# Performance work log

Hardware: AMD Instinct MI355X
Metric: run time of the kernel (lower is better)

Reference implementation:

```python
import jax, jax.numpy as jnp
import numpy as np

ALPHA, BETA, LAMB = 1.0, 1.0, 1e-4
K, TAU, DELTA = 16, 0.1, 1e-4
N, D, B, NQ = 100000, 256, 256, 4096


def setup_inputs() -> dict:
    key = jax.random.key(0)
    k1, k2, k3, k4, k5, k6 = jax.random.split(key, 6)
    X = jax.random.normal(k1, (N, D), dtype=jnp.float32)
    W = jax.random.normal(k2, (D, D), dtype=jnp.float32) / np.sqrt(D)
    q_batch = jax.random.normal(k3, (B, D), dtype=jnp.float32)
    pre_weights = jax.random.uniform(k4, (NQ, K), dtype=jnp.float32)
    pre_weights = pre_weights / pre_weights.sum(axis=1, keepdims=True)
    q_indices = jax.random.randint(k5, (B,), 0, NQ)
    pre_indices = jax.random.randint(k6, (NQ, K), 0, N)
    return {"X": X, "W": W, "q_batch": q_batch, "pre_weights": pre_weights,
            "q_indices": q_indices, "pre_indices": pre_indices}


def _matrix_sqrt(A):
    # differentiable symmetric matrix sqrt via eigendecomposition
    w, v = jnp.linalg.eigh(A)
    w = jnp.sqrt(jnp.clip(w, 0.0))
    return (v * w) @ v.T


def _loss_dist(T, mu_X, cov_X, cov_X_sqrt):
    mu = jnp.mean(T, axis=0)
    Tc = T - mu
    cov = Tc.T @ Tc / T.shape[0] + DELTA * jnp.eye(T.shape[1], dtype=T.dtype)
    loss_mean = jnp.sum((mu - mu_X) ** 2)
    cov_sqrt = _matrix_sqrt(cov)
    sqrt_term = _matrix_sqrt(cov_sqrt @ cov_X @ cov_sqrt)
    loss_cov = jnp.trace(cov_X + cov - 2.0 * sqrt_term)
    return jnp.clip(loss_mean + loss_cov, 0.0)


def _kl_per_sample(pre_idx, pre_w, post_idx, post_w):
    # union via first-occurrence mask over concatenated candidates [2K]
    cand = jnp.concatenate([pre_idx, post_idx])
    eq = cand[:, None] == cand[None, :]
    first = ~jnp.tril(eq, k=-1).any(axis=1)
    p = (cand[:, None] == pre_idx[None, :]).astype(pre_w.dtype) @ pre_w
    q = (cand[:, None] == post_idx[None, :]).astype(post_w.dtype) @ post_w
    p = jnp.where(first, jnp.clip(p, 1e-8), 0.0)
    p = p / p.sum()
    q = jnp.where(first, jnp.clip(q, 1e-8), 0.0)
    q = q / q.sum()
    logp = jnp.log(jnp.where(first, p, 1.0))
    logq = jnp.log(jnp.where(first, q, 1.0))
    return jnp.sum(jnp.where(first, p * (logp - logq), 0.0))


def _forward(X, W, q_batch, pre_weights, q_indices, pre_indices):
    # precomputed database stats
    mu_X = jnp.mean(X, axis=0)
    Xc = X - mu_X
    cov_X = Xc.T @ Xc / X.shape[0] + DELTA * jnp.eye(X.shape[1], dtype=X.dtype)
    cov_X_sqrt = _matrix_sqrt(cov_X)

    T = q_batch @ W  # model(q_batch): [B, D]

    loss_dist = _loss_dist(T, mu_X, cov_X, cov_X_sqrt)

    # brute-force exact KNN (faiss flat L2) on detached T
    Td = jax.lax.stop_gradient(T)
    d2 = (jnp.sum(Td * Td, axis=1, keepdims=True)
          - 2.0 * (Td @ X.T) + jnp.sum(X * X, axis=1))  # [B, N]
    _, post_idx = jax.lax.top_k(-d2, K)  # [B, K]

    X_nb = X[post_idx]  # [B, K, D]
    l2 = jnp.sum((T[:, None, :] - X_nb) ** 2, axis=-1)  # [B, K], with grad
    post_w = jax.nn.softmax(-l2 / TAU, axis=1)

    pre_idx_b = pre_indices[q_indices]   # [B, K]
    pre_w_b = pre_weights[q_indices]     # [B, K]
    kls = jax.vmap(_kl_per_sample)(pre_idx_b, pre_w_b, post_idx, post_w)
    loss_knn = jnp.mean(kls)

    loss_reg = 0.5 * jnp.sum(W ** 2)

    total = ALPHA * loss_dist + BETA * loss_knn + LAMB * loss_reg
    return total, loss_dist, loss_knn


def reference(X, W, q_batch, pre_weights, q_indices, pre_indices):
    return _forward(X, W, q_batch, pre_weights, q_indices, pre_indices)
```

## Files before the change

### kernel.cpp

```cpp
#include <hip/hip_runtime.h>

#define NPTS   100000
#define DIMD   256
#define BQ     256
#define PCHUNK 128
#define NPCH   782
#define NCAND  (NPCH*16)
#define NS_ITERS 26
#define KSPLIT  32
#define KSLICE  3136
#define KS2    576
#define NZ2    175

#define SC_LM   0
#define SC_TRCX 1
#define SC_TRCT 2
#define SC_FROB 3
#define SC_KNN  4
#define SC_REG  5
#define SC_LD   6

#define BIGF 3.4e38f

typedef __attribute__((ext_vector_type(4))) float f32x4;
typedef __attribute__((ext_vector_type(8))) unsigned short u16x8;
typedef __attribute__((ext_vector_type(8))) __bf16 bf16x8;

static __device__ __forceinline__ unsigned short f2bf(float f) {
    unsigned u = __float_as_uint(f);
    unsigned r = (u + 0x7fffu + ((u >> 16) & 1u)) >> 16;
    return (unsigned short)r;
}
static __device__ __forceinline__ float bf2f(unsigned short h) {
    return __uint_as_float(((unsigned)h) << 16);
}
static __device__ __forceinline__ unsigned pack_hi(float a, float b) {
    return (__float_as_uint(a) >> 16) | (__float_as_uint(b) & 0xffff0000u);
}
static __device__ __forceinline__ float trunc_bf(float a) {
    return __uint_as_float(__float_as_uint(a) & 0xffff0000u);
}
static __device__ __forceinline__ unsigned short top16(float v) {
    return (unsigned short)(__float_as_uint(v) >> 16);
}
static __device__ __forceinline__ f32x4 mfma16(u16x8 a, u16x8 b, f32x4 c) {
    return __builtin_amdgcn_mfma_f32_16x16x32_bf16(
        __builtin_bit_cast(bf16x8, a), __builtin_bit_cast(bf16x8, b), c, 0, 0, 0);
}

static __device__ __forceinline__ unsigned enc_f32(float f) {
    unsigned u = __float_as_uint(f);
    return u ^ (unsigned)(((int)u >> 31) | 0x80000000);
}
static __device__ __forceinline__ float dec_f32(unsigned e) {
    unsigned u = e ^ ((e & 0x80000000u) ? 0x80000000u : 0xFFFFFFFFu);
    return __uint_as_float(u);
}
static __device__ __forceinline__ unsigned umin32(unsigned a, unsigned b) { return a < b ? a : b; }
static __device__ __forceinline__ void ceu(unsigned& a, unsigned& b) {
    unsigned lo = a < b ? a : b;
    unsigned hi = a < b ? b : a;
    a = lo; b = hi;
}
static __device__ __forceinline__ void sort16(unsigned* r) {
#pragma unroll
    for (int k = 2; k <= 16; k <<= 1)
#pragma unroll
        for (int j = k >> 1; j > 0; j >>= 1)
#pragma unroll
            for (int i = 0; i < 16; ++i) {
                int l = i ^ j;
                if (l > i) {
                    if ((i & k) == 0) ceu(r[i], r[l]);
                    else              ceu(r[l], r[i]);
                }
            }
}
static __device__ __forceinline__ void clean16(unsigned* r) {
#pragma unroll
    for (int j = 8; j > 0; j >>= 1)
#pragma unroll
        for (int i = 0; i < 16; ++i) {
            int l = i ^ j;
            if (l > i) ceu(r[i], r[l]);
        }
}

__global__ __launch_bounds__(256) void zero_kernel(float* ws) {
    int idx = blockIdx.x * 256 + threadIdx.x;
    if (idx < 66560) ws[idx] = 0.0f;
}

__global__ __launch_bounds__(256) void statsx_kernel(const float* __restrict__ X,
                                                     float* __restrict__ xsq,
                                                     float* __restrict__ mu_sum,
                                                     unsigned short* __restrict__ XHs,
                                                     unsigned short* __restrict__ XLs) {
    int w    = threadIdx.x >> 6;
    int lane = threadIdx.x & 63;
    int rbase = blockIdx.x * 512;
    float cs0 = 0.f, cs1 = 0.f, cs2 = 0.f, cs3 = 0.f;
    for (int m = 0; m < 128; ++m) {
        int r = rbase + w + 4 * m;
        if (r < NPTS) {
            float4 v = *(const float4*)&X[r * DIMD + 4 * lane];
            cs0 += v.x; cs1 += v.y; cs2 += v.z; cs3 += v.w;
            float ss = v.x * v.x + v.y * v.y + v.z * v.z + v.w * v.w;
            for (int off = 32; off; off >>= 1) ss += __shfl_down(ss, off);
            if (lane == 0) xsq[r] = ss;
            if (XHs) {
                int g = (lane >> 1) ^ (r & 7);
                int h = lane & 1;
                uint2 hv = { pack_hi(v.x, v.y), pack_hi(v.z, v.w) };
                uint2 lv = { pack_hi(v.x - trunc_bf(v.x), v.y - trunc_bf(v.y)),
                             pack_hi(v.z - trunc_bf(v.z), v.w - trunc_bf(v.w)) };
                *(uint2*)(XHs + (size_t)r * 256 + g * 8 + h * 4) = hv;
                *(uint2*)(XLs + (size_t)r * 256 + g * 8 + h * 4) = lv;
            }
        } else if (XHs) {
            int g = (lane >> 1) ^ (r & 7);
            int h = lane & 1;
            uint2 z2 = {0u, 0u};
            *(uint2*)(XHs + (size_t)r * 256 + g * 8 + h * 4) = z2;
            *(uint2*)(XLs + (size_t)r * 256 + g * 8 + h * 4) = z2;
        }
    }
    atomicAdd(&mu_sum[4 * lane + 0], cs0);
    atomicAdd(&mu_sum[4 * lane + 1], cs1);
    atomicAdd(&mu_sum[4 * lane + 2], cs2);
    atomicAdd(&mu_sum[4 * lane + 3], cs3);
}

__global__ __launch_bounds__(256) void xtk_kernel(const unsigned short* __restrict__ XHs,
                                                  const unsigned short* __restrict__ XLs,
                                                  unsigned short* __restrict__ XTH,
                                                  unsigned short* __restrict__ XTL) {
    __shared__ unsigned short LH[32][268];
    __shared__ unsigned short LL[32][268];
    const int t = threadIdx.x;
#pragma unroll 1
    for (int st = 0; st < 8; ++st) {
        const int r0 = blockIdx.x * 256 + st * 32;
        const int row = t >> 3;
        const int r = r0 + row;
#pragma unroll
        for (int gg = 0; gg < 4; ++gg) {
            int glog = (t & 7) + gg * 8;
            int gphys = glog ^ (r & 7);
            u16x8 h = *(const u16x8*)(XHs + (size_t)r * 256 + gphys * 8);
            u16x8 l = *(const u16x8*)(XLs + (size_t)r * 256 + gphys * 8);
            *(u16x8*)&LH[row][glog * 8] = h;
            *(u16x8*)&LL[row][glog * 8] = l;
        }
        __syncthreads();
        {
            unsigned pk[16];
#pragma unroll
            for (int m = 0; m < 16; ++m)
                pk[m] = (unsigned)LH[2 * m][t] | ((unsigned)LH[2 * m + 1][t] << 16);
            uint4* oh = (uint4*)(XTH + (size_t)t * 100352 + r0);
#pragma unroll
            for (int q = 0; q < 4; ++q)
                oh[q] = make_uint4(pk[4 * q], pk[4 * q + 1], pk[4 * q + 2], pk[4 * q + 3]);
#pragma unroll
            for (int m = 0; m < 16; ++m)
                pk[m] = (unsigned)LL[2 * m][t] | ((unsigned)LL[2 * m + 1][t] << 16);
            uint4* ol = (uint4*)(XTL + (size_t)t * 100352 + r0);
#pragma unroll
            for (int q = 0; q < 4; ++q)
                ol[q] = make_uint4(pk[4 * q], pk[4 * q + 1], pk[4 * q + 2], pk[4 * q + 3]);
        }
        __syncthreads();
    }
}

__global__ __launch_bounds__(256) void covx2_kernel(const unsigned short* __restrict__ XTH,
                                                    const unsigned short* __restrict__ XTL,
                                                    float* __restrict__ acc_out) {
    const int quad = blockIdx.x;
    const int qi = quad >> 1, qj = quad & 1;
    const int t = threadIdx.x, w = t >> 6, lane = t & 63;
    const int l15 = lane & 15, l4 = lane >> 4;
    const int k0 = blockIdx.y * KS2;
    const int kend = (k0 + KS2 < 100352) ? (k0 + KS2) : 100352;
    f32x4 acc[2][8];
#pragma unroll
    for (int f = 0; f < 2; ++f)
#pragma unroll
        for (int cf = 0; cf < 8; ++cf) { f32x4 z = {0.f, 0.f, 0.f, 0.f}; acc[f][cf] = z; }
    const size_t rowA0 = (size_t)(qi * 128 + w * 32 + l15) * 100352;
    const size_t rowA1 = (size_t)(qi * 128 + w * 32 + 16 + l15) * 100352;
#pragma unroll 1
    for (int k = k0; k < kend; k += 32) {
        const int ko = k + l4 * 8;
        u16x8 ah0 = *(const u16x8*)(XTH + rowA0 + ko);
        u16x8 al0 = *(const u16x8*)(XTL + rowA0 + ko);
        u16x8 ah1 = *(const u16x8*)(XTH + rowA1 + ko);
        u16x8 al1 = *(const u16x8*)(XTL + rowA1 + ko);
#pragma unroll
        for (int cf = 0; cf < 8; ++cf) {
            const size_t rb = (size_t)(qj * 128 + cf * 16 + l15) * 100352 + ko;
            u16x8 bh = *(const u16x8*)(XTH + rb);
            u16x8 bl = *(const u16x8*)(XTL + rb);
            acc[0][cf] = mfma16(ah0, bh, acc[0][cf]);
            acc[0][cf] = mfma16(ah0, bl, acc[0][cf]);
            acc[0][cf] = mfma16(al0, bh, acc[0][cf]);
            acc[1][cf] = mfma16(ah1, bh, acc[1][cf]);
            acc[1][cf] = mfma16(ah1, bl, acc[1][cf]);
            acc[1][cf] = mfma16(al1, bh, acc[1][cf]);
        }
    }
#pragma unroll
    for (int f = 0; f < 2; ++f)
#pragma unroll
        for (int cf = 0; cf < 8; ++cf)
#pragma unroll
            for (int i = 0; i < 4; ++i) {
                const int r = qi * 128 + w * 32 + f * 16 + l4 * 4 + i;
                const int c = qj * 128 + cf * 16 + l15;
                atomicAdd(&acc_out[r * DIMD + c], acc[f][cf][i]);
            }
}

__global__ __launch_bounds__(256) void covx_kernel(const float* __restrict__ X,
                                                   float* __restrict__ acc_out) {
    __shared__ float Ais[16][64];
    __shared__ float Ajs[16][64];
    int t = threadIdx.x;
    int i0 = blockIdx.x * 64, j0 = blockIdx.y * 64;
    int ks = blockIdx.z * KSLICE;
    int lr = t >> 4, lc = (t & 15) * 4;
    int tx = t & 15, ty = t >> 4;
    float acc[4][4] = {};
    for (int kb = 0; kb < KSLICE; kb += 16) {
        int k = ks + kb + lr;
        if (k < NPTS) {
            float4 vi = *(const float4*)&X[k * DIMD + i0 + lc];
            float4 vj = *(const float4*)&X[k * DIMD + j0 + lc];
            *(float4*)&Ais[lr][lc] = vi;
            *(float4*)&Ajs[lr][lc] = vj;
        } else {
            float4 z = {0.f, 0.f, 0.f, 0.f};
            *(float4*)&Ais[lr][lc] = z;
            *(float4*)&Ajs[lr][lc] = z;
        }
        __syncthreads();
#pragma unroll
        for (int kk = 0; kk < 16; ++kk) {
            float4 a = *(float4*)&Ais[kk][tx * 4];
            float4 b = *(float4*)&Ajs[kk][ty * 4];
            float av[4] = {a.x, a.y, a.z, a.w};
            float bv[4] = {b.x, b.y, b.z, b.w};
#pragma unroll
            for (int m = 0; m < 4; ++m)
#pragma unroll
                for (int n = 0; n < 4; ++n) acc[m][n] += av[m] * bv[n];
        }
        __syncthreads();
    }
#pragma unroll
    for (int m = 0; m < 4; ++m)
#pragma unroll
        for (int n = 0; n < 4; ++n)
            atomicAdd(&acc_out[(i0 + 4 * tx + m) * DIMD + j0 + 4 * ty + n], acc[m][n]);
}

__global__ __launch_bounds__(256) void covxfin2_kernel(const float* __restrict__ acc,
                                                       const float* __restrict__ mu_sum,
                                                       float* __restrict__ covXf,
                                                       float* __restrict__ scal) {
    int idx = blockIdx.x * 256 + threadIdx.x;
    int i = idx >> 8, j = idx & 255;
    const float invN = 1.0f / (float)NPTS;
    float v = acc[idx] * invN - (mu_sum[i] * invN) * (mu_sum[j] * invN) + ((i == j) ? 1e-4f : 0.0f);
    covXf[idx] = v;
    if (i == j) atomicAdd(&scal[SC_TRCX], v);
}

__global__ __launch_bounds__(256) void mm32_kernel(const float* A, const float* B, float* C, const float* D,
                                                   const float* A2, const float* B2, float* C2, const float* D2,
                                                   int mode, const float* mu, float* scal) {
    __shared__ float As[32][32];
    __shared__ float Bs[32][32];
    __shared__ float red[256];
    int t = threadIdx.x;
    int tx = t & 15, ty = t >> 4;
    int i0 = blockIdx.x * 32, j0 = blockIdx.y * 32;
    int lr = t >> 3, lc = (t & 7) * 4;
    float acc[2][2] = {};
    for (int kb = 0; kb < 256; kb += 32) {
        if (mode == 2) {
            float4 v = *(const float4*)&A[(kb + lr) * DIMD + i0 + lc];
            *(float4*)&As[lr][lc] = v;
        } else {
            float4 v = *(const float4*)&A[(i0 + lr) * DIMD + kb + lc];
            As[lc + 0][lr] = v.x; As[lc + 1][lr] = v.y; As[lc + 2][lr] = v.z; As[lc + 3][lr] = v.w;
        }
        {
            float4 v = *(const float4*)&B[(kb + lr) * DIMD + j0 + lc];
            *(float4*)&Bs[lr][lc] = v;
        }
        __syncthreads();
#pragma unroll
        for (int kk = 0; kk < 32; ++kk) {
            float a0 = As[kk][2 * tx], a1 = As[kk][2 * tx + 1];
            float b0 = Bs[kk][2 * ty], b1 = Bs[kk][2 * ty + 1];
            acc[0][0] += a0 * b0; acc[0][1] += a0 * b1;
            acc[1][0] += a1 * b0; acc[1][1] += a1 * b1;
        }
        __syncthreads();
    }
    float fr = 0.f;
#pragma unroll
    for (int ii = 0; ii < 2; ++ii)
#pragma unroll
        for (int jj = 0; jj < 2; ++jj) {
            int i = i0 + 2 * tx + ii, j = j0 + 2 * ty + jj;
            float v = acc[ii][jj];
            if (mode == 2) {
                v = v * (1.0f / 256.0f) - mu[i] * mu[j] + ((i == j) ? 1e-4f : 0.0f);
                if (i == j) atomicAdd(&scal[SC_TRCT], v);
            }
            C[i * DIMD + j] = v;
            if (mode == 1) fr += v * v;
        }
    if (mode == 0 && C2 != nullptr) {
        unsigned short* TH = (unsigned short*)C2;
        unsigned short* TL = (unsigned short*)const_cast<float*>(D2);
#pragma unroll
        for (int ii = 0; ii < 2; ++ii) {
            int i = i0 + 2 * tx + ii;
            int jc = j0 + 2 * ty;
            float x0 = acc[ii][0], x1 = acc[ii][1];
            *(unsigned*)&TH[i * DIMD + jc] = pack_hi(x0, x1);
            *(unsigned*)&TL[i * DIMD + jc] = pack_hi(x0 - trunc_bf(x0), x1 - trunc_bf(x1));
        }
    }
    if (mode == 1) {
        red[t] = fr; __syncthreads();
        for (int s2 = 128; s2 > 0; s2 >>= 1) { if (t < s2) red[t] += red[t + s2]; __syncthreads(); }
        if (t == 0) atomicAdd(&scal[SC_FROB], red[0]);
    }
}

__global__ __launch_bounds__(256) void tstats_kernel(const float* __restrict__ Tm,
                                                     const float* __restrict__ mu_sum,
                                                     float* __restrict__ mu_T,
                                                     float* __restrict__ scal) {
    __shared__ float red[256];
    int j = threadIdx.x;
    float s = 0.f;
    for (int b = 0; b < BQ; ++b) s += Tm[b * DIMD + j];
    float mt = s * (1.0f / 256.0f);
    mu_T[j] = mt;
    float d = mt - mu_sum[j] * (1.0f / (float)NPTS);
    red[j] = d * d;
    __syncthreads();
    for (int s2 = 128; s2 > 0; s2 >>= 1) { if (j < s2) red[j] += red[j + s2]; __syncthreads(); }
    if (j == 0) scal[SC_LM] = red[0];
}

__global__ __launch_bounds__(256) void inityz2_kernel(const float* __restrict__ G,
                                                      const float* __restrict__ scal,
                                                      float* __restrict__ Y, float* __restrict__ Z,
                                                      unsigned short* __restrict__ YaH,
                                                      unsigned short* __restrict__ YaL,
                                                      unsigned short* __restrict__ ZaH,
                                                      unsigned short* __restrict__ ZaL) {
    int idx = blockIdx.x * 256 + threadIdx.x;
    float invs = rsqrtf(scal[SC_FROB]);
    float y = G[idx] * invs;
    Y[idx] = y;
    YaH[idx] = top16(y);
    YaL[idx] = top16(y - trunc_bf(y));
    bool dg = ((idx >> 8) == (idx & 255));
    Z[idx] = dg ? 1.0f : 0.0f;
    ZaH[idx] = dg ? (unsigned short)0x3F80 : (unsigned short)0;
    ZaL[idx] = 0;
}

__global__ __launch_bounds__(256) void nsfused_kernel(
        const float* __restrict__ Ycur, const float* __restrict__ Zcur,
        const unsigned short* __restrict__ YH, const unsigned short* __restrict__ YL,
        const unsigned short* __restrict__ ZH, const unsigned short* __restrict__ ZL,
        float* __restrict__ Yn, float* __restrict__ Zn,
        unsigned short* __restrict__ YnH, unsigned short* __restrict__ YnL,
        unsigned short* __restrict__ ZnH, unsigned short* __restrict__ ZnL) {
    __shared__ __align__(16) unsigned short VH[32 * 264];
    __shared__ __align__(16) unsigned short VL[32 * 264];
    __shared__ __align__(16) unsigned short IH[32 * 264];
    __shared__ __align__(16) unsigned short IL[32 * 264];
    const int t = threadIdx.x, w = t >> 6, lane = t & 63;
    const int l15 = lane & 15, l4 = lane >> 4;
    const int j0 = blockIdx.x * 32;
    const unsigned short *M1H, *M1L, *M2H, *M2L, *VsH, *VsL;
    const float* Dm; float* Out; unsigned short *OH, *OL;
    if (blockIdx.y == 0) { M1H = ZH; M1L = ZL; M2H = YH; M2L = YL; VsH = YH; VsL = YL;
                           Dm = Ycur; Out = Yn; OH = YnH; OL = YnL; }
    else                 { M1H = YH; M1L = YL; M2H = ZH; M2L = ZL; VsH = ZH; VsL = ZL;
                           Dm = Zcur; Out = Zn; OH = ZnH; OL = ZnL; }
    {
        const int col = t & 31, k0 = (t >> 5) * 32;
#pragma unroll
        for (int m = 0; m < 16; ++m) {
            const int k = k0 + 2 * m;
            unsigned h0 = VsH[(size_t)k * 256 + j0 + col];
            unsigned h1 = VsH[(size_t)(k + 1) * 256 + j0 + col];
            unsigned l0 = VsL[(size_t)k * 256 + j0 + col];
            unsigned l1 = VsL[(size_t)(k + 1) * 256 + j0 + col];
            *(unsigned*)&VH[col * 264 + k] = h0 | (h1 << 16);
            *(unsigned*)&VL[col * 264 + k] = l0 | (l1 << 16);
        }
    }
    __syncthreads();
    f32x4 acc[4][2];
#pragma unroll
    for (int f = 0; f < 4; ++f)
#pragma unroll
        for (int cf = 0; cf < 2; ++cf) { f32x4 z = {0.f, 0.f, 0.f, 0.f}; acc[f][cf] = z; }
#pragma unroll
    for (int ks = 0; ks < 8; ++ks) {
        const int bo0 = l15 * 264 + ks * 32 + l4 * 8;
        const int bo1 = (16 + l15) * 264 + ks * 32 + l4 * 8;
        u16x8 bh0 = *(const u16x8*)&VH[bo0];
        u16x8 bl0 = *(const u16x8*)&VL[bo0];
        u16x8 bh1 = *(const u16x8*)&VH[bo1];
        u16x8 bl1 = *(const u16x8*)&VL[bo1];
#pragma unroll
        for (int f = 0; f < 4; ++f) {
            const size_t ro = (size_t)(w * 64 + f * 16 + l15) * 256 + ks * 32 + l4 * 8;
            u16x8 ah = *(const u16x8*)(M1H + ro);
            u16x8 al = *(const u16x8*)(M1L + ro);
            acc[f][0] = mfma16(ah, bh0, acc[f][0]);
            acc[f][0] = mfma16(ah, bl0, acc[f][0]);
            acc[f][0] = mfma16(al, bh0, acc[f][0]);
            acc[f][1] = mfma16(ah, bh1, acc[f][1]);
            acc[f][1] = mfma16(ah, bl1, acc[f][1]);
            acc[f][1] = mfma16(al, bh1, acc[f][1]);
        }
    }
#pragma unroll
    for (int f = 0; f < 4; ++f)
#pragma unroll
        for (int cf = 0; cf < 2; ++cf) {
            float v0 = acc[f][cf][0], v1 = acc[f][cf][1], v2 = acc[f][cf][2], v3 = acc[f][cf][3];
            unsigned h01 = pack_hi(v0, v1), h23 = pack_hi(v2, v3);
            unsigned l01 = pack_hi(v0 - trunc_bf(v0), v1 - trunc_bf(v1));
            unsigned l23 = pack_hi(v2 - trunc_bf(v2), v3 - trunc_bf(v3));
            const int ad = (cf * 16 + l15) * 264 + w * 64 + f * 16 + l4 * 4;
            *(uint2*)&IH[ad] = make_uint2(h01, h23);
            *(uint2*)&IL[ad] = make_uint2(l01, l23);
        }
    __syncthreads();
#pragma unroll
    for (int f = 0; f < 4; ++f)
#pragma unroll
        for (int cf = 0; cf < 2; ++cf) { f32x4 z = {0.f, 0.f, 0.f, 0.f}; acc[f][cf] = z; }
#pragma unroll
    for (int ks = 0; ks < 8; ++ks) {
        const int bo0 = l15 * 264 + ks * 32 + l4 * 8;
        const int bo1 = (16 + l15) * 264 + ks * 32 + l4 * 8;
        u16x8 bh0 = *(const u16x8*)&IH[bo0];
        u16x8 bl0 = *(const u16x8*)&IL[bo0];
        u16x8 bh1 = *(const u16x8*)&IH[bo1];
        u16x8 bl1 = *(const u16x8*)&IL[bo1];
#pragma unroll
        for (int f = 0; f < 4; ++f) {
            const size_t ro = (size_t)(w * 64 + f * 16 + l15) * 256 + ks * 32 + l4 * 8;
            u16x8 ah = *(const u16x8*)(M2H + ro);
            u16x8 al = *(const u16x8*)(M2L + ro);
            acc[f][0] = mfma16(ah, bh0, acc[f][0]);
            acc[f][0] = mfma16(ah, bl0, acc[f][0]);
            acc[f][0] = mfma16(al, bh0, acc[f][0]);
            acc[f][1] = mfma16(ah, bh1, acc[f][1]);
            acc[f][1] = mfma16(ah, bl1, acc[f][1]);
            acc[f][1] = mfma16(al, bh1, acc[f][1]);
        }
    }
#pragma unroll
    for (int f = 0; f < 4; ++f)
#pragma unroll
        for (int cf = 0; cf < 2; ++cf)
#pragma unroll
            for (int i = 0; i < 4; ++i) {
                const int r = w * 64 + f * 16 + l4 * 4 + i;
                const int c = j0 + cf * 16 + l15;
                float v = 1.5f * Dm[r * 256 + c] - 0.5f * acc[f][cf][i];
                Out[r * 256 + c] = v;
                OH[r * 256 + c] = top16(v);
                OL[r * 256 + c] = top16(v - trunc_bf(v));
            }
}

__global__ __launch_bounds__(256) void findist_kernel(const float* __restrict__ Yfin,
                                                      float* __restrict__ scal) {
    __shared__ float red[256];
    int t = threadIdx.x;
    red[t] = Yfin[t * (DIMD + 1)];
    __syncthreads();
    for (int s2 = 128; s2 > 0; s2 >>= 1) { if (t < s2) red[t] += red[t + s2]; __syncthreads(); }
    if (t == 0) {
        float frobsq = scal[SC_FROB];
        float tr_sqrt = powf(frobsq, 0.25f) * red[0];
        float lc = scal[SC_TRCX] + scal[SC_TRCT] - 2.0f * tr_sqrt;
        scal[SC_LD] = fmaxf(0.0f, scal[SC_LM] + lc);
    }
}

__global__ __launch_bounds__(256) void reg_kernel(const float* __restrict__ W, float* __restrict__ scal) {
    __shared__ float red[256];
    int t = threadIdx.x;
    float s = 0.f;
    int base = blockIdx.x * 1024;
    for (int m = 0; m < 4; ++m) { float w = W[base + m * 256 + t]; s += w * w; }
    red[t] = s;
    __syncthreads();
    for (int s2 = 128; s2 > 0; s2 >>= 1) { if (t < s2) red[t] += red[t + s2]; __syncthreads(); }
    if (t == 0) atomicAdd(&scal[SC_REG], red[0]);
}

__global__ __launch_bounds__(256, 2) void knn3_kernel(const unsigned short* __restrict__ TmH,
                                                      const unsigned short* __restrict__ TmL,
                                                      const unsigned short* __restrict__ XHs,
                                                      const unsigned short* __restrict__ XLs,
                                                      const float* __restrict__ xsq,
                                                      float* __restrict__ ck, int* __restrict__ ci) {
    __shared__ __align__(16) unsigned char sm2[69632];
    unsigned* kt = (unsigned*)(sm2 + 32768);
    const int t = threadIdx.x;
    const int w = t >> 6, lane = t & 63;
    const int l15 = lane & 15, l4 = lane >> 4;
    const int p0 = blockIdx.x * PCHUNK;
    const int swz = (l15 & 7) << 4;

    unsigned sk[16];
#pragma unroll
    for (int s = 0; s < 16; ++s) sk[s] = 0xFFFFFFFFu;

    uint4 ph[4], pl[4];
    {
        const uint4* gh = (const uint4*)(XHs + (size_t)p0 * 256);
        const uint4* gl = (const uint4*)(XLs + (size_t)p0 * 256);
#pragma unroll
        for (int r = 0; r < 4; ++r) { ph[r] = gh[r * 256 + t]; pl[r] = gl[r * 256 + t]; }
    }

#pragma unroll 1
    for (int pc = 0; pc < 4; ++pc) {
        const int pbase = p0 + pc * 32;
#pragma unroll
        for (int r = 0; r < 4; ++r) {
            *(uint4*)(sm2 + (r * 256 + t) * 16) = ph[r];
            *(uint4*)(sm2 + 16384 + (r * 256 + t) * 16) = pl[r];
        }
        __syncthreads();
        f32x4 acc[4][2];
#pragma unroll
        for (int f = 0; f < 4; ++f)
#pragma unroll
            for (int pt = 0; pt < 2; ++pt) { f32x4 z = {0.f, 0.f, 0.f, 0.f}; acc[f][pt] = z; }
#pragma unroll
        for (int ks = 0; ks < 8; ++ks) {
            const int g = (((ks * 4 + l4) << 4)) ^ swz;
            const int b0 = l15 * 512 + g;
            const int b1 = (16 + l15) * 512 + g;
            u16x8 bh0 = *(const u16x8*)(sm2 + b0);
            u16x8 bl0 = *(const u16x8*)(sm2 + 16384 + b0);
            u16x8 bh1 = *(const u16x8*)(sm2 + b1);
            u16x8 bl1 = *(const u16x8*)(sm2 + 16384 + b1);
#pragma unroll
            for (int f = 0; f < 4; ++f) {
                const size_t ro = (size_t)(w * 64 + f * 16 + l15) * 256 + ks * 32 + l4 * 8;
                u16x8 ah = *(const u16x8*)(TmH + ro);
                u16x8 al = *(const u16x8*)(TmL + ro);
                acc[f][0] = mfma16(ah, bh0, acc[f][0]);
                acc[f][0] = mfma16(ah, bl0, acc[f][0]);
                acc[f][0] = mfma16(al, bh0, acc[f][0]);
                acc[f][1] = mfma16(ah, bh1, acc[f][1]);
                acc[f][1] = mfma16(ah, bl1, acc[f][1]);
                acc[f][1] = mfma16(al, bh1, acc[f][1]);
            }
        }
#pragma unroll
        for (int pt = 0; pt < 2; ++pt) {
            const int p = pbase + pt * 16 + l15;
            const float xv = xsq[p];
            const bool ok = (p < NPTS);
            const unsigned lidx = (unsigned)(pc * 32 + pt * 16 + l15);
#pragma unroll
            for (int f = 0; f < 4; ++f)
#pragma unroll
                for (int i = 0; i < 4; ++i) {
                    float d2 = ok ? (xv - 2.0f * acc[f][pt][i]) : BIGF;
                    unsigned e = (enc_f32(d2) & 0xFFFFFF80u) | lidx;
                    kt[(w * 64 + f * 16 + l4 * 4 + i) * 36 + pt * 16 + l15] = e;
                }
        }
        __syncthreads();
        if (pc < 3) {
            const uint4* gh = (const uint4*)(XHs + (size_t)(p0 + (pc + 1) * 32) * 256);
            const uint4* gl = (const uint4*)(XLs + (size_t)(p0 + (pc + 1) * 32) * 256);
#pragma unroll
            for (int r = 0; r < 4; ++r) { ph[r] = gh[r * 256 + t]; pl[r] = gl[r * 256 + t]; }
        }
        {
            unsigned b[32];
#pragma unroll
            for (int c4 = 0; c4 < 8; ++c4) {
                uint4 v = *(const uint4*)(kt + t * 36 + c4 * 4);
                b[c4 * 4 + 0] = v.x; b[c4 * 4 + 1] = v.y;
                b[c4 * 4 + 2] = v.z; b[c4 * 4 + 3] = v.w;
            }
            sort16(b);
            sort16(b + 16);
#pragma unroll
            for (int i = 0; i < 16; ++i) b[i] = umin32(b[i], b[31 - i]);
            clean16(b);
#pragma unroll
            for (int i = 0; i < 16; ++i) sk[i] = umin32(sk[i], b[15 - i]);
            clean16(sk);
        }
    }
    const int base = t * NCAND + blockIdx.x * 16;
#pragma unroll
    for (int s = 0; s < 16; ++s) {
        ck[base + s] = dec_f32(sk[s] & 0xFFFFFF80u);
        ci[base + s] = p0 + (int)(sk[s] & 127u);
    }
}

static __device__ __forceinline__ void knn_load(const float* __restrict__ X, int p0, int pc, int t,
                                                float4 s0[2], float4 s1[2]) {
#pragma unroll
    for (int rep = 0; rep < 2; ++rep) {
        int g = t + rep * 512;
        int row = g >> 5, c0 = (g & 31) * 8;
        int p = p0 + pc * 32 + row;
        if (p < NPTS) {
            s0[rep] = *(const float4*)&X[p * DIMD + c0];
            s1[rep] = *(const float4*)&X[p * DIMD + c0 + 4];
        } else {
            float4 z = {0.f, 0.f, 0.f, 0.f};
            s0[rep] = z; s1[rep] = z;
        }
    }
}
static __device__ __forceinline__ void knn_write(unsigned short* XH, unsigned short* XL, int t,
                                                 const float4 s0[2], const float4 s1[2]) {
#pragma unroll
    for (int rep = 0; rep < 2; ++rep) {
        int g = t + rep * 512;
        int row = g >> 5, c0 = (g & 31) * 8;
        float f[8] = {s0[rep].x, s0[rep].y, s0[rep].z, s0[rep].w,
                      s1[rep].x, s1[rep].y, s1[rep].z, s1[rep].w};
        u16x8 h, lo;
#pragma unroll
        for (int j = 0; j < 8; ++j) {
            unsigned short hb = f2bf(f[j]);
            h[j] = hb;
            lo[j] = f2bf(f[j] - bf2f(hb));
        }
        *(u16x8*)&XH[row * 264 + c0] = h;
        *(u16x8*)&XL[row * 264 + c0] = lo;
    }
}
__global__ __launch_bounds__(512, 2) void knn_kernel(const float* __restrict__ Tm,
                                                     const float* __restrict__ X,
                                                     const float* __restrict__ xsq,
                                                     float* __restrict__ ck, int* __restrict__ ci) {
    __shared__ __align__(16) unsigned char smem[50688];
    unsigned short* XH = (unsigned short*)smem;
    unsigned short* XL = (unsigned short*)(smem + 16896);
    float* ktf = (float*)smem;
    float* tk  = (float*)(smem + 34304);
    int*   ti  = (int*)  (smem + 42496);
    const int t    = threadIdx.x;
    const int w    = t >> 6;
    const int lane = t & 63;
    const int l15  = lane & 15;
    const int l4   = lane >> 4;
    const int p0   = blockIdx.x * PCHUNK;
    const int q0   = blockIdx.y * 128;
    u16x8 aH[8], aL[8];
    {
        const int q = q0 + w * 16 + l15;
        const float* tq = Tm + q * DIMD + l4 * 8;
#pragma unroll
        for (int ks = 0; ks < 8; ++ks) {
            float4 v0 = *(const float4*)(tq + ks * 32);
            float4 v1 = *(const float4*)(tq + ks * 32 + 4);
            float f[8] = {v0.x, v0.y, v0.z, v0.w, v1.x, v1.y, v1.z, v1.w};
            u16x8 h, lo;
#pragma unroll
            for (int j = 0; j < 8; ++j) {
                unsigned short hb = f2bf(f[j]);
                h[j] = hb;
                lo[j] = f2bf(f[j] - bf2f(hb));
            }
            aH[ks] = h; aL[ks] = lo;
        }
    }
    float worst = BIGF; int wslot = 0;
    float4 s0[2], s1[2];
    knn_load(X, p0, 0, t, s0, s1);
    knn_write(XH, XL, t, s0, s1);
#pragma unroll
    for (int h = 0; h < 2; ++h) {
        f32x4 acc[4];
#pragma unroll
        for (int a2 = 0; a2 < 4; ++a2) { f32x4 z = {0.f, 0.f, 0.f, 0.f}; acc[a2] = z; }
#pragma unroll
        for (int pc2 = 0; pc2 < 2; ++pc2) {
            const int pc = 2 * h + pc2;
            __syncthreads();
            if (pc < 3) knn_load(X, p0, pc + 1, t, s0, s1);
#pragma unroll
            for (int ks = 0; ks < 8; ++ks) {
#pragma unroll
                for (int pt = 0; pt < 2; ++pt) {
                    const int off = (pt * 16 + l15) * 264 + ks * 32 + l4 * 8;
                    u16x8 bh = *(const u16x8*)&XH[off];
                    u16x8 bl = *(const u16x8*)&XL[off];
                    acc[pc2 * 2 + pt] = mfma16(aH[ks], bh, acc[pc2 * 2 + pt]);
                    acc[pc2 * 2 + pt] = mfma16(aH[ks], bl, acc[pc2 * 2 + pt]);
                    acc[pc2 * 2 + pt] = mfma16(aL[ks], bh, acc[pc2 * 2 + pt]);
                }
            }
            __syncthreads();
            if (pc2 == 0 && pc < 3) knn_write(XH, XL, t, s0, s1);
        }
#pragma unroll
        for (int pc2 = 0; pc2 < 2; ++pc2) {
#pragma unroll
            for (int pt = 0; pt < 2; ++pt) {
                const int pl = pc2 * 32 + pt * 16 + l15;
                const int p  = p0 + h * 64 + pl;
                const float xv = (p < NPTS) ? xsq[p] : 0.f;
#pragma unroll
                for (int i = 0; i < 4; ++i) {
                    float key = (p < NPTS) ? (xv - 2.0f * acc[pc2 * 2 + pt][i]) : BIGF;
                    ktf[(w * 16 + l4 * 4 + i) * 67 + pl] = key;
                }
            }
        }
        __syncthreads();
        if (t < 128) {
            if (h == 0) {
#pragma unroll
                for (int s = 0; s < 16; ++s) { tk[s * 128 + t] = BIGF; ti[s * 128 + t] = 0x7fffffff; }
            }
            for (int c = 0; c < 64; ++c) {
                float key = ktf[t * 67 + c];
                if (key < worst) {
                    tk[wslot * 128 + t] = key; ti[wslot * 128 + t] = p0 + h * 64 + c;
                    worst = tk[t]; wslot = 0;
#pragma unroll
                    for (int s = 1; s < 16; ++s) {
                        float v = tk[s * 128 + t];
                        if (v > worst) { worst = v; wslot = s; }
                    }
                }
            }
        }
        __syncthreads();
        if (h == 0) knn_write(XH, XL, t, s0, s1);
    }
    if (t < 128) {
        int base = (q0 + t) * NCAND + blockIdx.x * 16;
        for (int s = 0; s < 16; ++s) { ck[base + s] = tk[s * 128 + t]; ci[base + s] = ti[s * 128 + t]; }
    }
}

__global__ __launch_bounds__(256) void merge_kernel(const float* __restrict__ ck,
                                                    const int* __restrict__ ci,
                                                    int* __restrict__ post_idx) {
    __shared__ float tk[16][256];
    __shared__ int   ti[16][256];
    __shared__ float rk[256];
    __shared__ int   ri[256];
    __shared__ int   rt2[256];
    __shared__ int   rs2[256];
    int q = blockIdx.x, t = threadIdx.x;
    for (int s = 0; s < 16; ++s) { tk[s][t] = BIGF; ti[s][t] = 0x7fffffff; }
    float worst = BIGF; int wslot = 0;
    for (int e = t; e < NCAND; e += 256) {
        float key = ck[q * NCAND + e];
        if (key < worst) {
            tk[wslot][t] = key; ti[wslot][t] = ci[q * NCAND + e];
            worst = tk[0][t]; wslot = 0;
            for (int s = 1; s < 16; ++s)
                if (tk[s][t] > worst) { worst = tk[s][t]; wslot = s; }
        }
    }
    __syncthreads();
    for (int r = 0; r < 16; ++r) {
        float bk = tk[0][t]; int bi = ti[0][t], bs = 0;
        for (int s = 1; s < 16; ++s) {
            float k2 = tk[s][t]; int i2 = ti[s][t];
            if (k2 < bk || (k2 == bk && i2 < bi)) { bk = k2; bi = i2; bs = s; }
        }
        rk[t] = bk; ri[t] = bi; rt2[t] = t; rs2[t] = bs;
        __syncthreads();
        for (int s2 = 128; s2 > 0; s2 >>= 1) {
            if (t < s2) {
                float ko = rk[t + s2]; int io = ri[t + s2];
                if (ko < rk[t] || (ko == rk[t] && io < ri[t])) {
                    rk[t] = ko; ri[t] = io; rt2[t] = rt2[t + s2]; rs2[t] = rs2[t + s2];
                }
            }
            __syncthreads();
        }
        if (t == rt2[0]) { tk[rs2[0]][t] = BIGF; ti[rs2[0]][t] = 0x7fffffff; }
        if (t == 0) post_idx[q * 16 + r] = ri[0];
        __syncthreads();
    }
}

__global__ __launch_bounds__(256) void l2sm_kernel(const float* __restrict__ Tm,
                                                   const float* __restrict__ X,
                                                   const int* __restrict__ post_idx,
                                                   float* __restrict__ post_w) {
    __shared__ float l2s[16];
    int b = blockIdx.x, t = threadIdx.x;
    int k = t >> 4, j = t & 15;
    int idx = post_idx[b * 16 + k];
    float s = 0.f;
    for (int i = 0; i < 16; ++i) {
        int d = j + 16 * i;
        float df = Tm[b * DIMD + d] - X[idx * DIMD + d];
        s += df * df;
    }
    for (int off = 8; off; off >>= 1) s += __shfl_down(s, off, 16);
    if (j == 0) l2s[k] = s;
    __syncthreads();
    if (t < 16) {
        float x = -l2s[t] * 10.0f;
        float m = x;
        for (int mm = 8; mm; mm >>= 1) m = fmaxf(m, __shfl_xor(m, mm, 16));
        float e = expf(x - m);
        float ssum = e;
        for (int mm = 8; mm; mm >>= 1) ssum += __shfl_xor(ssum, mm, 16);
        post_w[b * 16 + t] = e / ssum;
    }
}

__global__ __launch_bounds__(256) void kl_kernel(const int* __restrict__ q_indices,
                                                 const int* __restrict__ pre_indices,
                                                 const float* __restrict__ pre_weights,
                                                 const int* __restrict__ post_idx,
                                                 const float* __restrict__ post_w,
                                                 float* __restrict__ scal) {
    int b = threadIdx.x;
    int qi = q_indices[b];
    int pid[16]; float pw[16]; int sid[16]; float sw[16];
    for (int k = 0; k < 16; ++k) {
        pid[k] = pre_indices[qi * 16 + k];
        pw[k]  = pre_weights[qi * 16 + k];
        sid[k] = post_idx[b * 16 + k];
        sw[k]  = post_w[b * 16 + k];
    }
    float psum = 0.f, qsum = 0.f, kl = 0.f;
    for (int pass = 0; pass < 2; ++pass) {
        for (int i = 0; i < 32; ++i) {
            int c = (i < 16) ? pid[i] : sid[i - 16];
            bool first = true;
            for (int jj = 0; jj < i; ++jj) {
                int cj = (jj < 16) ? pid[jj] : sid[jj - 16];
                if (cj == c) { first = false; break; }
            }
            if (!first) continue;
            float p = 0.f, q = 0.f;
            for (int k2 = 0; k2 < 16; ++k2) {
                if (pid[k2] == c) p += pw[k2];
                if (sid[k2] == c) q += sw[k2];
            }
            p = fmaxf(p, 1e-8f); q = fmaxf(q, 1e-8f);
            if (pass == 0) { psum += p; qsum += q; }
            else {
                float pn = p / psum, qn = q / qsum;
                kl += pn * (logf(pn) - logf(qn));
            }
        }
    }
    atomicAdd(&scal[SC_KNN], kl * (1.0f / 256.0f));
}

__global__ void assemble_kernel(const float* __restrict__ scal, float* __restrict__ out) {
    if (threadIdx.x == 0) {
        float ld = scal[SC_LD], lk = scal[SC_KNN], reg = scal[SC_REG];
        out[0] = ld + lk + 1e-4f * 0.5f * reg;
        out[1] = ld;
        out[2] = lk;
    }
}

extern "C" void kernel_launch(void* const* d_in, const int* in_sizes, int n_in,
                              void* d_out, int out_size, void* d_ws, size_t ws_size,
                              hipStream_t stream) {
    (void)in_sizes; (void)n_in; (void)out_size;
    const float* X           = (const float*)d_in[0];
    const float* W           = (const float*)d_in[1];
    const float* q_batch     = (const float*)d_in[2];
    const float* pre_weights = (const float*)d_in[3];
    const int*   q_indices   = (const int*)d_in[4];
    const int*   pre_indices = (const int*)d_in[5];
    float* out = (float*)d_out;
    float* ws  = (float*)d_ws;

    float* mu_sum = ws + 0;
    float* scal   = ws + 256;
    float* mu_T   = ws + 512;
    float* covX   = ws + 1024;
    float* Tm     = ws + 66560;
    float* cov    = ws + 132096;
    float* G      = ws + 197632;
    float* Ya     = ws + 263168;
    float* Za     = ws + 328704;
    float* Yb     = ws + 394240;
    float* Zb     = ws + 459776;
    float* covXf  = ws + 525312;
    float* xsq    = ws + 590848;
    float* post_w = ws + 691200;
    int*   post_idx = (int*)(ws + 695296);
    float* ck     = ws + 699392;
    int*   ci     = (int*)(ws + 3902464);
    unsigned short* YaH = (unsigned short*)(ws + 699392);
    unsigned short* YaL = (unsigned short*)(ws + 732160);
    unsigned short* ZaH = (unsigned short*)(ws + 764928);
    unsigned short* ZaL = (unsigned short*)(ws + 797696);
    unsigned short* YbH = (unsigned short*)(ws + 830464);
    unsigned short* YbL = (unsigned short*)(ws + 863232);
    unsigned short* ZbH = (unsigned short*)(ws + 896000);
    unsigned short* ZbL = (unsigned short*)(ws + 928768);
    unsigned short* XHs = (unsigned short*)(ws + 7105536);
    unsigned short* XLs = (unsigned short*)(ws + 19950592);
    unsigned short* TmH = (unsigned short*)(ws + 32795648);
    unsigned short* TmL = (unsigned short*)(ws + 32828416);
    unsigned short* XTH = (unsigned short*)(ws + 32845824);
    unsigned short* XTL = (unsigned short*)(ws + 45690880);
    const bool haveIMG = (ws_size >= (size_t)131444736);
    const bool haveXT  = (ws_size >= (size_t)234143744);

    zero_kernel<<<260, 256, 0, stream>>>(ws);
    reg_kernel<<<64, 256, 0, stream>>>(W, scal);
    statsx_kernel<<<196, 256, 0, stream>>>(X, xsq, mu_sum,
                                           haveIMG ? XHs : nullptr, haveIMG ? XLs : nullptr);
    if (haveXT) {
        xtk_kernel<<<392, 256, 0, stream>>>(XHs, XLs, XTH, XTL);
        covx2_kernel<<<dim3(4, NZ2), 256, 0, stream>>>(XTH, XTL, covX);
    } else {
        covx_kernel<<<dim3(4, 4, KSPLIT), 256, 0, stream>>>(X, covX);
    }
    covxfin2_kernel<<<256, 256, 0, stream>>>(covX, mu_sum, covXf, scal);
    mm32_kernel<<<dim3(8, 8, 1), 256, 0, stream>>>(q_batch, W, Tm, nullptr,
                                                   nullptr, nullptr,
                                                   haveIMG ? (float*)TmH : nullptr,
                                                   haveIMG ? (float*)TmL : nullptr, 0, nullptr, scal);
    tstats_kernel<<<1, 256, 0, stream>>>(Tm, mu_sum, mu_T, scal);
    mm32_kernel<<<dim3(8, 8, 1), 256, 0, stream>>>(Tm, Tm, cov, nullptr,
                                                   nullptr, nullptr, nullptr, nullptr, 2, mu_T, scal);
    mm32_kernel<<<dim3(8, 8, 1), 256, 0, stream>>>(cov, covXf, G, nullptr,
                                                   nullptr, nullptr, nullptr, nullptr, 1, nullptr, scal);
    if (haveIMG) {
        knn3_kernel<<<NPCH, 256, 0, stream>>>(TmH, TmL, XHs, XLs, xsq, ck, ci);
    } else {
        knn_kernel<<<dim3(NPCH, 2, 1), 512, 0, stream>>>(Tm, X, xsq, ck, ci);
    }
    merge_kernel<<<256, 256, 0, stream>>>(ck, ci, post_idx);
    l2sm_kernel<<<256, 256, 0, stream>>>(Tm, X, post_idx, post_w);
    kl_kernel<<<1, 256, 0, stream>>>(q_indices, pre_indices, pre_weights, post_idx, post_w, scal);
    inityz2_kernel<<<256, 256, 0, stream>>>(G, scal, Ya, Za, YaH, YaL, ZaH, ZaL);
    {
        float *Yc = Ya, *Zc = Za, *Yn = Yb, *Zn = Zb;
        unsigned short *cYH = YaH, *cYL = YaL, *cZH = ZaH, *cZL = ZaL;
        unsigned short *nYH = YbH, *nYL = YbL, *nZH = ZbH, *nZL = ZbL;
        for (int it = 0; it < NS_ITERS; ++it) {
            nsfused_kernel<<<dim3(8, 2), 256, 0, stream>>>(Yc, Zc, cYH, cYL, cZH, cZL,
                                                           Yn, Zn, nYH, nYL, nZH, nZL);
            float* tf;
            tf = Yc; Yc = Yn; Yn = tf;
            tf = Zc; Zc = Zn; Zn = tf;
            unsigned short* tu;
            tu = cYH; cYH = nYH; nYH = tu;
            tu = cYL; cYL = nYL; nYL = tu;
            tu = cZH; cZH = nZH; nZH = tu;
            tu = cZL; cZL = nZL; nZL = tu;
        }
        findist_kernel<<<1, 256, 0, stream>>>(Yc, scal);
    }
    assemble_kernel<<<1, 64, 0, stream>>>(scal, out);
}
```

Baseline: 1.704 ms.

## Rework statsx, Newton-Schulz, knn3 tiling and add per-query merge kernel

Splits statsx over four times more blocks, halves the column tile of the fused Newton-Schulz kernel so it launches 32 blocks instead of 16, and changes knn3 to load X tiles directly instead of register-prefetching them. knn3 now also sorts its 32 candidate keys as two separate 16-element halves merged into the running top-16. A new merge2 kernel runs one block per query, doing a per-thread insertion top-16 followed by a shared-memory tree reduction. The aim is more parallelism on the latency-bound small kernels, but knn3 loses its load/compute overlap and merge2 depends on early exit in the sorted runs.

```diff
diff --git a/kernel.cpp b/kernel.cpp
--- a/kernel.cpp
+++ b/kernel.cpp
@@ -85,6 +85,24 @@
             if (l > i) ceu(r[i], r[l]);
         }
 }
+static __device__ __forceinline__ int lessp(float ka, int ia, float kb, int ib) {
+    return (ka < kb) || (ka == kb && ia < ib);
+}
+static __device__ __forceinline__ void ceup(float& ka, int& ia, float& kb, int& ib) {
+    bool sw = lessp(kb, ib, ka, ia);
+    float t0 = sw ? kb : ka, t1 = sw ? ka : kb;
+    int   u0 = sw ? ib : ia, u1 = sw ? ia : ib;
+    ka = t0; kb = t1; ia = u0; ib = u1;
+}
+static __device__ __forceinline__ void cleanp16(float* k, int* i) {
+#pragma unroll
+    for (int j = 8; j > 0; j >>= 1)
+#pragma unroll
+        for (int x = 0; x < 16; ++x) {
+            int l = x ^ j;
+            if (l > x) ceup(k[x], i[x], k[l], i[l]);
+        }
+}
 
 __global__ __launch_bounds__(256) void zero_kernel(float* ws) {
     int idx = blockIdx.x * 256 + threadIdx.x;
@@ -98,9 +116,9 @@
                                                      unsigned short* __restrict__ XLs) {
     int w    = threadIdx.x >> 6;
     int lane = threadIdx.x & 63;
-    int rbase = blockIdx.x * 512;
+    int rbase = blockIdx.x * 128;
     float cs0 = 0.f, cs1 = 0.f, cs2 = 0.f, cs3 = 0.f;
-    for (int m = 0; m < 128; ++m) {
+    for (int m = 0; m < 32; ++m) {
         int r = rbase + w + 4 * m;
         if (r < NPTS) {
             float4 v = *(const float4*)&X[r * DIMD + 4 * lane];
@@ -386,13 +404,13 @@
         float* __restrict__ Yn, float* __restrict__ Zn,
         unsigned short* __restrict__ YnH, unsigned short* __restrict__ YnL,
         unsigned short* __restrict__ ZnH, unsigned short* __restrict__ ZnL) {
-    __shared__ __align__(16) unsigned short VH[32 * 264];
-    __shared__ __align__(16) unsigned short VL[32 * 264];
-    __shared__ __align__(16) unsigned short IH[32 * 264];
-    __shared__ __align__(16) unsigned short IL[32 * 264];
+    __shared__ __align__(16) unsigned short VH[16 * 264];
+    __shared__ __align__(16) unsigned short VL[16 * 264];
+    __shared__ __align__(16) unsigned short IH[16 * 264];
+    __shared__ __align__(16) unsigned short IL[16 * 264];
     const int t = threadIdx.x, w = t >> 6, lane = t & 63;
     const int l15 = lane & 15, l4 = lane >> 4;
-    const int j0 = blockIdx.x * 32;
+    const int j0 = blockIdx.x * 16;
     const unsigned short *M1H, *M1L, *M2H, *M2L, *VsH, *VsL;
     const float* Dm; float* Out; unsigned short *OH, *OL;
     if (blockIdx.y == 0) { M1H = ZH; M1L = ZL; M2H = YH; M2L = YL; VsH = YH; VsL = YL;
@@ -400,9 +418,9 @@
     else                 { M1H = YH; M1L = YL; M2H = ZH; M2L = ZL; VsH = ZH; VsL = ZL;
                            Dm = Zcur; Out = Zn; OH = ZnH; OL = ZnL; }
     {
-        const int col = t & 31, k0 = (t >> 5) * 32;
-#pragma unroll
-        for (int m = 0; m < 16; ++m) {
+        const int col = t >> 4, k0 = (t & 15) * 16;
+#pragma unroll
+        for (int m = 0; m < 8; ++m) {
             const int k = k0 + 2 * m;
             unsigned h0 = VsH[(size_t)k * 256 + j0 + col];
             unsigned h1 = VsH[(size_t)(k + 1) * 256 + j0 + col];
@@ -413,83 +431,63 @@
         }
     }
     __syncthreads();
-    f32x4 acc[4][2];
-#pragma unroll
-    for (int f = 0; f < 4; ++f)
-#pragma unroll
-        for (int cf = 0; cf < 2; ++cf) { f32x4 z = {0.f, 0.f, 0.f, 0.f}; acc[f][cf] = z; }
+    f32x4 acc[4];
+#pragma unroll
+    for (int f = 0; f < 4; ++f) { f32x4 z = {0.f, 0.f, 0.f, 0.f}; acc[f] = z; }
 #pragma unroll
     for (int ks = 0; ks < 8; ++ks) {
-        const int bo0 = l15 * 264 + ks * 32 + l4 * 8;
-        const int bo1 = (16 + l15) * 264 + ks * 32 + l4 * 8;
-        u16x8 bh0 = *(const u16x8*)&VH[bo0];
-        u16x8 bl0 = *(const u16x8*)&VL[bo0];
-        u16x8 bh1 = *(const u16x8*)&VH[bo1];
-        u16x8 bl1 = *(const u16x8*)&VL[bo1];
+        const int bo = l15 * 264 + ks * 32 + l4 * 8;
+        u16x8 bh = *(const u16x8*)&VH[bo];
+        u16x8 bl = *(const u16x8*)&VL[bo];
 #pragma unroll
         for (int f = 0; f < 4; ++f) {
             const size_t ro = (size_t)(w * 64 + f * 16 + l15) * 256 + ks * 32 + l4 * 8;
             u16x8 ah = *(const u16x8*)(M1H + ro);
             u16x8 al = *(const u16x8*)(M1L + ro);
-            acc[f][0] = mfma16(ah, bh0, acc[f][0]);
-            acc[f][0] = mfma16(ah, bl0, acc[f][0]);
-            acc[f][0] = mfma16(al, bh0, acc[f][0]);
-            acc[f][1] = mfma16(ah, bh1, acc[f][1]);
-            acc[f][1] = mfma16(ah, bl1, acc[f][1]);
-            acc[f][1] = mfma16(al, bh1, acc[f][1]);
-        }
-    }
-#pragma unroll
-    for (int f = 0; f < 4; ++f)
-#pragma unroll
-        for (int cf = 0; cf < 2; ++cf) {
-            float v0 = acc[f][cf][0], v1 = acc[f][cf][1], v2 = acc[f][cf][2], v3 = acc[f][cf][3];
-            unsigned h01 = pack_hi(v0, v1), h23 = pack_hi(v2, v3);
-            unsigned l01 = pack_hi(v0 - trunc_bf(v0), v1 - trunc_bf(v1));
-            unsigned l23 = pack_hi(v2 - trunc_bf(v2), v3 - trunc_bf(v3));
-            const int ad = (cf * 16 + l15) * 264 + w * 64 + f * 16 + l4 * 4;
-            *(uint2*)&IH[ad] = make_uint2(h01, h23);
-            *(uint2*)&IL[ad] = make_uint2(l01, l23);
-        }
+            acc[f] = mfma16(ah, bh, acc[f]);
+            acc[f] = mfma16(ah, bl, acc[f]);
+            acc[f] = mfma16(al, bh, acc[f]);
+        }
+    }
+#pragma unroll
+    for (int f = 0; f < 4; ++f) {
+        float v0 = acc[f][0], v1 = acc[f][1], v2 = acc[f][2], v3 = acc[f][3];
+        unsigned h01 = pack_hi(v0, v1), h23 = pack_hi(v2, v3);
+        unsigned l01 = pack_hi(v0 - trunc_bf(v0), v1 - trunc_bf(v1));
+        unsigned l23 = pack_hi(v2 - trunc_bf(v2), v3 - trunc_bf(v3));
+        const int ad = l15 * 264 + w * 64 + f * 16 + l4 * 4;
+        *(uint2*)&IH[ad] = make_uint2(h01, h23);
+        *(uint2*)&IL[ad] = make_uint2(l01, l23);
+    }
     __syncthreads();
 #pragma unroll
-    for (int f = 0; f < 4; ++f)
-#pragma unroll
-        for (int cf = 0; cf < 2; ++cf) { f32x4 z = {0.f, 0.f, 0.f, 0.f}; acc[f][cf] = z; }
+    for (int f = 0; f < 4; ++f) { f32x4 z = {0.f, 0.f, 0.f, 0.f}; acc[f] = z; }
 #pragma unroll
     for (int ks = 0; ks < 8; ++ks) {
-        const int bo0 = l15 * 264 + ks * 32 + l4 * 8;
-        const int bo1 = (16 + l15) * 264 + ks * 32 + l4 * 8;
-        u16x8 bh0 = *(const u16x8*)&IH[bo0];
-        u16x8 bl0 = *(const u16x8*)&IL[bo0];
-        u16x8 bh1 = *(const u16x8*)&IH[bo1];
-        u16x8 bl1 = *(const u16x8*)&IL[bo1];
+        const int bo = l15 * 264 + ks * 32 + l4 * 8;
+        u16x8 bh = *(const u16x8*)&IH[bo];
+        u16x8 bl = *(const u16x8*)&IL[bo];
 #pragma unroll
         for (int f = 0; f < 4; ++f) {
             const size_t ro = (size_t)(w * 64 + f * 16 + l15) * 256 + ks * 32 + l4 * 8;
             u16x8 ah = *(const u16x8*)(M2H + ro);
             u16x8 al = *(const u16x8*)(M2L + ro);
-            acc[f][0] = mfma16(ah, bh0, acc[f][0]);
-            acc[f][0] = mfma16(ah, bl0, acc[f][0]);
-            acc[f][0] = mfma16(al, bh0, acc[f][0]);
-            acc[f][1] = mfma16(ah, bh1, acc[f][1]);
-            acc[f][1] = mfma16(ah, bl1, acc[f][1]);
-            acc[f][1] = mfma16(al, bh1, acc[f][1]);
+            acc[f] = mfma16(ah, bh, acc[f]);
+            acc[f] = mfma16(ah, bl, acc[f]);
+            acc[f] = mfma16(al, bh, acc[f]);
         }
     }
 #pragma unroll
     for (int f = 0; f < 4; ++f)
 #pragma unroll
-        for (int cf = 0; cf < 2; ++cf)
-#pragma unroll
-            for (int i = 0; i < 4; ++i) {
-                const int r = w * 64 + f * 16 + l4 * 4 + i;
-                const int c = j0 + cf * 16 + l15;
-                float v = 1.5f * Dm[r * 256 + c] - 0.5f * acc[f][cf][i];
-                Out[r * 256 + c] = v;
-                OH[r * 256 + c] = top16(v);
-                OL[r * 256 + c] = top16(v - trunc_bf(v));
-            }
+        for (int i = 0; i < 4; ++i) {
+            const int r = w * 64 + f * 16 + l4 * 4 + i;
+            const int c = j0 + l15;
+            float v = 1.5f * Dm[r * 256 + c] - 0.5f * acc[f][i];
+            Out[r * 256 + c] = v;
+            OH[r * 256 + c] = top16(v);
+            OL[r * 256 + c] = top16(v - trunc_bf(v));
+        }
 }
 
 __global__ __launch_bounds__(256) void findist_kernel(const float* __restrict__ Yfin,
@@ -537,21 +535,19 @@
 #pragma unroll
     for (int s = 0; s < 16; ++s) sk[s] = 0xFFFFFFFFu;
 
-    uint4 ph[4], pl[4];
-    {
-        const uint4* gh = (const uint4*)(XHs + (size_t)p0 * 256);
-        const uint4* gl = (const uint4*)(XLs + (size_t)p0 * 256);
-#pragma unroll
-        for (int r = 0; r < 4; ++r) { ph[r] = gh[r * 256 + t]; pl[r] = gl[r * 256 + t]; }
-    }
-
 #pragma unroll 1
     for (int pc = 0; pc < 4; ++pc) {
         const int pbase = p0 + pc * 32;
-#pragma unroll
-        for (int r = 0; r < 4; ++r) {
-            *(uint4*)(sm2 + (r * 256 + t) * 16) = ph[r];
-            *(uint4*)(sm2 + 16384 + (r * 256 + t) * 16) = pl[r];
+        {
+            const uint4* gh = (const uint4*)(XHs + (size_t)pbase * 256);
+            const uint4* gl = (const uint4*)(XLs + (size_t)pbase * 256);
+#pragma unroll
+            for (int r = 0; r < 4; ++r) {
+                uint4 vh = gh[r * 256 + t];
+                uint4 vl = gl[r * 256 + t];
+                *(uint4*)(sm2 + (r * 256 + t) * 16) = vh;
+                *(uint4*)(sm2 + 16384 + (r * 256 + t) * 16) = vl;
+            }
         }
         __syncthreads();
         f32x4 acc[4][2];
@@ -597,25 +593,16 @@
                 }
         }
         __syncthreads();
-        if (pc < 3) {
-            const uint4* gh = (const uint4*)(XHs + (size_t)(p0 + (pc + 1) * 32) * 256);
-            const uint4* gl = (const uint4*)(XLs + (size_t)(p0 + (pc + 1) * 32) * 256);
-#pragma unroll
-            for (int r = 0; r < 4; ++r) { ph[r] = gh[r * 256 + t]; pl[r] = gl[r * 256 + t]; }
-        }
-        {
-            unsigned b[32];
-#pragma unroll
-            for (int c4 = 0; c4 < 8; ++c4) {
-                uint4 v = *(const uint4*)(kt + t * 36 + c4 * 4);
+#pragma unroll
+        for (int hb = 0; hb < 2; ++hb) {
+            unsigned b[16];
+#pragma unroll
+            for (int c4 = 0; c4 < 4; ++c4) {
+                uint4 v = *(const uint4*)(kt + t * 36 + hb * 16 + c4 * 4);
                 b[c4 * 4 + 0] = v.x; b[c4 * 4 + 1] = v.y;
                 b[c4 * 4 + 2] = v.z; b[c4 * 4 + 3] = v.w;
             }
             sort16(b);
-            sort16(b + 16);
-#pragma unroll
-            for (int i = 0; i < 16; ++i) b[i] = umin32(b[i], b[31 - i]);
-            clean16(b);
 #pragma unroll
             for (int i = 0; i < 16; ++i) sk[i] = umin32(sk[i], b[15 - i]);
             clean16(sk);
@@ -768,6 +755,63 @@
     if (t < 128) {
         int base = (q0 + t) * NCAND + blockIdx.x * 16;
         for (int s = 0; s < 16; ++s) { ck[base + s] = tk[s * 128 + t]; ci[base + s] = ti[s * 128 + t]; }
+    }
+}
+
+__global__ __launch_bounds__(256) void merge2_kernel(const float* __restrict__ ck,
+                                                     const int* __restrict__ ci,
+                                                     int* __restrict__ post_idx) {
+    __shared__ float km[16 * 256];
+    __shared__ int   im[16 * 256];
+    const int q = blockIdx.x, t = threadIdx.x;
+    float sk[16]; int si[16];
+#pragma unroll
+    for (int s = 0; s < 16; ++s) { sk[s] = BIGF; si[s] = 0x7fffffff; }
+#pragma unroll 1
+    for (int run = t; run < NPCH; run += 256) {
+        const float* rk = ck + (size_t)q * NCAND + run * 16;
+        const int*   ri = ci + (size_t)q * NCAND + run * 16;
+#pragma unroll 1
+        for (int s = 0; s < 16; ++s) {
+            float k = rk[s]; int id = ri[s];
+            if (!lessp(k, id, sk[15], si[15])) break;
+#pragma unroll
+            for (int j = 15; j > 0; --j) {
+                bool a = lessp(k, id, sk[j - 1], si[j - 1]);
+                bool b = lessp(k, id, sk[j], si[j]);
+                float nk = a ? sk[j - 1] : (b ? k : sk[j]);
+                int   ni = a ? si[j - 1] : (b ? id : si[j]);
+                sk[j] = nk; si[j] = ni;
+            }
+            bool c = lessp(k, id, sk[0], si[0]);
+            float nk0 = c ? k : sk[0]; int ni0 = c ? id : si[0];
+            sk[0] = nk0; si[0] = ni0;
+        }
+    }
+#pragma unroll
+    for (int s = 0; s < 16; ++s) { km[s * 256 + t] = sk[s]; im[s * 256 + t] = si[s]; }
+    __syncthreads();
+    for (int off = 128; off > 0; off >>= 1) {
+        if (t < off) {
+            float bk[16]; int bi[16];
+#pragma unroll
+            for (int s = 0; s < 16; ++s) { bk[s] = km[s * 256 + t + off]; bi[s] = im[s * 256 + t + off]; }
+#pragma unroll
+            for (int s = 0; s < 16; ++s) {
+                float ak = sk[s];  int ai = si[s];
+                float ok = bk[15 - s]; int oi = bi[15 - s];
+                bool a = lessp(ak, ai, ok, oi);
+                sk[s] = a ? ak : ok; si[s] = a ? ai : oi;
+            }
+            cleanp16(sk, si);
+#pragma unroll
+            for (int s = 0; s < 16; ++s) { km[s * 256 + t] = sk[s]; im[s * 256 + t] = si[s]; }
+        }
+        __syncthreads();
+    }
+    if (t == 0) {
+#pragma unroll
+        for (int r = 0; r < 16; ++r) post_idx[q * 16 + r] = si[r];
     }
 }
 
@@ -943,7 +987,7 @@
 
     zero_kernel<<<260, 256, 0, stream>>>(ws);
     reg_kernel<<<64, 256, 0, stream>>>(W, scal);
-    statsx_kernel<<<196, 256, 0, stream>>>(X, xsq, mu_sum,
+    statsx_kernel<<<784, 256, 0, stream>>>(X, xsq, mu_sum,
                                            haveIMG ? XHs : nullptr, haveIMG ? XLs : nullptr);
     if (haveXT) {
         xtk_kernel<<<392, 256, 0, stream>>>(XHs, XLs, XTH, XTL);
@@ -963,10 +1007,11 @@
                                                    nullptr, nullptr, nullptr, nullptr, 1, nullptr, scal);
     if (haveIMG) {
         knn3_kernel<<<NPCH, 256, 0, stream>>>(TmH, TmL, XHs, XLs, xsq, ck, ci);
+        merge2_kernel<<<256, 256, 0, stream>>>(ck, ci, post_idx);
     } else {
         knn_kernel<<<dim3(NPCH, 2, 1), 512, 0, stream>>>(Tm, X, xsq, ck, ci);
-    }
-    merge_kernel<<<256, 256, 0, stream>>>(ck, ci, post_idx);
+        merge_kernel<<<256, 256, 0, stream>>>(ck, ci, post_idx);
+    }
     l2sm_kernel<<<256, 256, 0, stream>>>(Tm, X, post_idx, post_w);
     kl_kernel<<<1, 256, 0, stream>>>(q_indices, pre_indices, pre_weights, post_idx, post_w, scal);
     inityz2_kernel<<<256, 256, 0, stream>>>(G, scal, Ya, Za, YaH, YaL, ZaH, ZaL);
@@ -975,8 +1020,8 @@
         unsigned short *cYH = YaH, *cYL = YaL, *cZH = ZaH, *cZL = ZaL;
         unsigned short *nYH = YbH, *nYL = YbL, *nZH = ZbH, *nZL = ZbL;
         for (int it = 0; it < NS_ITERS; ++it) {
-            nsfused_kernel<<<dim3(8, 2), 256, 0, stream>>>(Yc, Zc, cYH, cYL, cZH, cZL,
-                                                           Yn, Zn, nYH, nYL, nZH, nZL);
+            nsfused_kernel<<<dim3(16, 2), 256, 0, stream>>>(Yc, Zc, cYH, cYL, cZH, cZL,
+                                                            Yn, Zn, nYH, nYL, nZH, nZL);
             float* tf;
             tf = Yc; Yc = Yn; Yn = tf;
             tf = Zc; Zc = Zn; Zn = tf;
```

Result: faster. 1.662 ms (-2.5%).
